# Optimization experiments

Measured on AMD Instinct MI355X. Metric: run time of the kernel, lower is better.

## Reference

```python
import jax, jax.numpy as jnp
import numpy as np

B, C, IMG = 128, 3, 224
P = 16
NP = (IMG // P) ** 2          # 196 patches
S = 1 + NP                    # 197 tokens
D = 384
HEADS = 6
HD = D // HEADS               # 64
DEPTH = 12
HID = 4 * D                   # 1536
NCLS = 100
PATCH_DIM = C * P * P         # 768
EPS = 1e-5


def setup_inputs() -> dict:
    key = jax.random.key(0)
    ks = jax.random.split(key, 24)
    g = lambda k, shape, s=0.02: jax.random.normal(k, shape, dtype=jnp.float32) * s
    return {
        "x": jax.random.normal(ks[0], (B, C, IMG, IMG), dtype=jnp.float32),
        "patch_w": g(ks[1], (D, PATCH_DIM)),
        "patch_b": jnp.zeros((D,), jnp.float32),
        "cls_token": g(ks[2], (1, 1, D)),
        "pos_embed": g(ks[3], (1, S, D)),
        "ln1_g": jnp.ones((DEPTH, D), jnp.float32),
        "ln1_b": jnp.zeros((DEPTH, D), jnp.float32),
        "qkv_w": g(ks[4], (DEPTH, 3 * D, D)),
        "qkv_b": jnp.zeros((DEPTH, 3 * D), jnp.float32),
        "out_w": g(ks[5], (DEPTH, D, D)),
        "out_b": jnp.zeros((DEPTH, D), jnp.float32),
        "ln2_g": jnp.ones((DEPTH, D), jnp.float32),
        "ln2_b": jnp.zeros((DEPTH, D), jnp.float32),
        "fc1_w": g(ks[6], (DEPTH, HID, D)),
        "fc1_b": jnp.zeros((DEPTH, HID), jnp.float32),
        "fc2_w": g(ks[7], (DEPTH, D, HID)),
        "fc2_b": jnp.zeros((DEPTH, D), jnp.float32),
        "lnf_g": jnp.ones((D,), jnp.float32),
        "lnf_b": jnp.zeros((D,), jnp.float32),
        "head_w": g(ks[8], (NCLS, D)),
    }


def _ln(x, g, b):
    m = jnp.mean(x, axis=-1, keepdims=True)
    v = jnp.mean(jnp.square(x - m), axis=-1, keepdims=True)
    return (x - m) * jax.lax.rsqrt(v + EPS) * g + b


def reference(x, patch_w, patch_b, cls_token, pos_embed,
              ln1_g, ln1_b, qkv_w, qkv_b, out_w, out_b,
              ln2_g, ln2_b, fc1_w, fc1_b, fc2_w, fc2_b,
              lnf_g, lnf_b, head_w):
    b = x.shape[0]
    hp = IMG // P
    # patchify: unfold(2,P).unfold(3,P).permute(0,2,3,1,4,5) -> [B, N, C*P*P]
    patches = x.reshape(b, C, hp, P, hp, P).transpose(0, 2, 4, 1, 3, 5).reshape(b, NP, PATCH_DIM)
    tok = patches @ patch_w.T + patch_b                           # [B, NP, D]
    h = jnp.concatenate([jnp.broadcast_to(cls_token, (b, 1, D)), tok], axis=1)
    h = h + pos_embed[:, :S, :]
    scale = 1.0 / np.sqrt(HD).astype(np.float32)
    for i in range(DEPTH):
        xn = _ln(h, ln1_g[i], ln1_b[i])
        qkv = xn @ qkv_w[i].T + qkv_b[i]                          # [B, S, 3D]
        q, k, v = jnp.split(qkv, 3, axis=-1)
        q = q.reshape(b, S, HEADS, HD).transpose(0, 2, 1, 3) * scale
        k = k.reshape(b, S, HEADS, HD).transpose(0, 2, 1, 3)
        v = v.reshape(b, S, HEADS, HD).transpose(0, 2, 1, 3)
        attn = jax.nn.softmax(jnp.einsum('bhqd,bhkd->bhqk', q, k), axis=-1)
        ctx = jnp.einsum('bhqk,bhkd->bhqd', attn, v)
        ctx = ctx.transpose(0, 2, 1, 3).reshape(b, S, D)
        h = h + (ctx @ out_w[i].T + out_b[i])
        xn2 = _ln(h, ln2_g[i], ln2_b[i])
        hid = jax.nn.gelu(xn2 @ fc1_w[i].T + fc1_b[i], approximate=False)
        h = h + (hid @ fc2_w[i].T + fc2_b[i])
    cls = _ln(h[:, 0], lnf_g, lnf_b)
    return cls @ head_w.T                                         # [B, NCLS]
```

## Files before the change

### kernel.cpp

```cpp
#include <hip/hip_runtime.h>
#include <hip/hip_bf16.h>


#define S_ 197
#define D_ 384
#define BATCH 128

using bf16 = __hip_bfloat16;
typedef __attribute__((ext_vector_type(8))) __bf16 bf16x8;
typedef __attribute__((ext_vector_type(4))) float f32x4;

#if __has_builtin(__builtin_amdgcn_global_load_lds)
#define HAVE_GLL 1
__device__ __forceinline__ void gll16(const bf16* g, __bf16* l) {
  __builtin_amdgcn_global_load_lds(
      (const __attribute__((address_space(1))) void*)g,
      (__attribute__((address_space(3))) void*)l, 16, 0, 0);
}
#else
#define HAVE_GLL 0
#endif

__global__ __launch_bounds__(256) void k_f2b(const float* __restrict__ src,
                                             bf16* __restrict__ dst, int n4) {
  int i = blockIdx.x * 256 + threadIdx.x;
  if (i >= n4) return;
  float4 v = ((const float4*)src)[i];
  bf16 o[4] = {__float2bfloat16(v.x), __float2bfloat16(v.y),
               __float2bfloat16(v.z), __float2bfloat16(v.w)};
  ((uint2*)dst)[i] = *(uint2*)o;
}

__global__ __launch_bounds__(256) void k_embed_init(const float* __restrict__ cls,
                                                    const float* __restrict__ pos,
                                                    float* __restrict__ h) {
  int idx = blockIdx.x * 256 + threadIdx.x;
  if (idx >= BATCH * S_ * D_) return;
  int d = idx % D_;
  int s = (idx / D_) % S_;
  float v = pos[s * D_ + d];
  if (s == 0) v += cls[d];
  h[idx] = v;
}

__global__ __launch_bounds__(256) void k_patchify(const float* __restrict__ x,
                                                  bf16* __restrict__ patches) {
  int idx = blockIdx.x * 256 + threadIdx.x;
  if (idx >= BATCH * 196 * 768) return;
  int f = idx % 768;
  int n = (idx / 768) % 196;
  int b = idx / (768 * 196);
  int c = f >> 8, rem = f & 255, dy = rem >> 4, dx = rem & 15;
  int py = n / 14, px = n % 14;
  patches[idx] = __float2bfloat16(
      x[(((size_t)b * 3 + c) * 224 + py * 16 + dy) * 224 + px * 16 + dx]);
}

template <int MODE>
__global__ __launch_bounds__(256, 6) void k_gemm(const bf16* __restrict__ X,
                                                 const bf16* __restrict__ W,
                                                 const float* __restrict__ bias,
                                                 bf16* __restrict__ out,
                                                 float* __restrict__ res,
                                                 int N, int K, int remap) {
  __shared__ __align__(16) __bf16 As[2][64 * 32];
  __shared__ __align__(16) __bf16 Bs[2][128 * 32];
  const int tid = threadIdx.x;
  const int m0 = blockIdx.y * 64, n0 = blockIdx.x * 128;
  const int lane = tid & 63, w = tid >> 6;
  const int l16 = lane & 15, quad = lane >> 4;
  f32x4 acc[4][2] = {};

  const int scol = (((lane & 3) ^ ((lane >> 3) & 3)) << 3);
  const bf16* Ag = X + (size_t)(m0 + w * 16 + (lane >> 2)) * K + scol;
  const bf16* Bg = W + (size_t)(n0 + w * 32 + (lane >> 2)) * K + scol;
  const int ldsA = w * 512;
  const int ldsB = w * 1024;

  const int jx8 = ((quad ^ ((l16 >> 1) & 3)) << 3);
  const int aoff = l16 * 32 + jx8;
  const int boff = (w * 32 + l16) * 32 + jx8;

#if HAVE_GLL
#define STAGE(buf, k0)                                       \
  do {                                                       \
    gll16(Ag + (k0), &As[buf][ldsA]);                        \
    gll16(Bg + (k0), &Bs[buf][ldsB]);                        \
    gll16(Bg + (k0) + (size_t)16 * K, &Bs[buf][ldsB + 512]); \
  } while (0)
#else
#define STAGE(buf, k0)                                                       \
  do {                                                                       \
    *(uint4*)(&As[buf][ldsA + (lane >> 2) * 32 + (lane & 3) * 8]) =          \
        *(const uint4*)(Ag + (k0) - scol + (lane & 3) * 8);                  \
    *(uint4*)(&Bs[buf][ldsB + (lane >> 2) * 32 + (lane & 3) * 8]) =          \
        *(const uint4*)(Bg + (k0) - scol + (lane & 3) * 8);                  \
    *(uint4*)(&Bs[buf][ldsB + 512 + (lane >> 2) * 32 + (lane & 3) * 8]) =    \
        *(const uint4*)(Bg + (k0) - scol + (size_t)16 * K + (lane & 3) * 8); \
  } while (0)
#endif

  STAGE(0, 0);
  __syncthreads();
  for (int k0 = 0; k0 < K; k0 += 32) {
    const int cb = (k0 >> 5) & 1;
    if (k0 + 32 < K) STAGE(cb ^ 1, k0 + 32);
    bf16x8 av[4], bv[2];
#pragma unroll
    for (int i = 0; i < 4; i++)
      av[i] = *(const bf16x8*)(&As[cb][aoff + i * 512]);
#pragma unroll
    for (int j = 0; j < 2; j++)
      bv[j] = *(const bf16x8*)(&Bs[cb][boff + j * 512]);
#pragma unroll
    for (int i = 0; i < 4; i++)
#pragma unroll
      for (int j = 0; j < 2; j++)
        acc[i][j] = __builtin_amdgcn_mfma_f32_16x16x32_bf16(av[i], bv[j], acc[i][j], 0, 0, 0);
    __syncthreads();
  }
#undef STAGE

  float bvv[2];
#pragma unroll
  for (int j = 0; j < 2; j++)
    bvv[j] = bias[n0 + w * 32 + j * 16 + l16];
#pragma unroll
  for (int i = 0; i < 4; i++) {
    const int rbase = m0 + i * 16 + quad * 4;
#pragma unroll
    for (int j = 0; j < 2; j++) {
      const int col = n0 + w * 32 + j * 16 + l16;
#pragma unroll
      for (int r = 0; r < 4; r++) {
        float v = acc[i][j][r] + bvv[j];
        int rw = rbase + r;
        if (MODE == 0) {
          out[(size_t)rw * N + col] = __float2bfloat16(v);
        } else if (MODE == 1) {
          float gl = 0.5f * v * (1.f + erff(v * 0.70710678118f));
          out[(size_t)rw * N + col] = __float2bfloat16(gl);
        } else {
          int hr = remap ? (rw + rw / 196 + 1) : rw;
          res[(size_t)hr * N + col] += v;
        }
      }
    }
  }
}

__global__ __launch_bounds__(128) void k_ln(const float* __restrict__ h,
                                            const float* __restrict__ g,
                                            const float* __restrict__ bt,
                                            bf16* __restrict__ xn) {
  const int r = blockIdx.x, t = threadIdx.x;
  const float* row = h + (size_t)r * D_;
  float x0 = row[t], x1 = row[t + 128], x2 = row[t + 256];
  float s = x0 + x1 + x2;
  float q = x0 * x0 + x1 * x1 + x2 * x2;
#pragma unroll
  for (int o = 32; o; o >>= 1) {
    s += __shfl_xor(s, o);
    q += __shfl_xor(q, o);
  }
  __shared__ float rs[2], rq[2];
  if ((t & 63) == 0) { rs[t >> 6] = s; rq[t >> 6] = q; }
  __syncthreads();
  s = rs[0] + rs[1];
  q = rq[0] + rq[1];
  const float mean = s * (1.f / 384.f);
  const float var = q * (1.f / 384.f) - mean * mean;
  const float rstd = rsqrtf(var + 1e-5f);
  bf16* o = xn + (size_t)r * D_;
  o[t] = __float2bfloat16((x0 - mean) * rstd * g[t] + bt[t]);
  o[t + 128] = __float2bfloat16((x1 - mean) * rstd * g[t + 128] + bt[t + 128]);
  o[t + 256] = __float2bfloat16((x2 - mean) * rstd * g[t + 256] + bt[t + 256]);
}

__global__ __launch_bounds__(256) void k_attn(const bf16* __restrict__ qkv,
                                              bf16* __restrict__ ctx) {
  const int bh = blockIdx.x;
  const int b = bh / 6, hd = bh % 6;
  const bf16* Qg = qkv + (size_t)b * S_ * 1152 + hd * 64;
  const bf16* Kg = Qg + 384;
  const bf16* Vg = Qg + 768;
  __shared__ __align__(16) __bf16 Vt[64 * 232];
  __shared__ __align__(16) __bf16 Ps[4][16 * 232];
  const int tid = threadIdx.x;
  const int lane = tid & 63, w = tid >> 6;
  const int l16 = lane & 15, quad = lane >> 4;
  const __bf16 z = (__bf16)0.0f;

  for (int i = tid; i < 64 * 35; i += 256) {
    int d = i / 35, k = 197 + i % 35;
    Vt[d * 232 + k] = z;
  }
  for (int i = tid; i < S_ * 64; i += 256) {
    int k = i >> 6, d = i & 63;
    Vt[d * 232 + k] = *(const __bf16*)&Vg[(size_t)k * 1152 + d];
  }
  for (int i = lane; i < 16 * 24; i += 64) {
    int r = i / 24, c = 208 + i % 24;
    Ps[w][r * 232 + c] = z;
  }
  __syncthreads();

  const bf16x8 zf = {};
  for (int band = w; band < 13; band += 4) {
    const int qrow = band * 16 + l16;
    bf16x8 aq0 = zf, aq1 = zf;
    if (qrow < S_) {
      aq0 = *(const bf16x8*)(Qg + (size_t)qrow * 1152 + quad * 8);
      aq1 = *(const bf16x8*)(Qg + (size_t)qrow * 1152 + 32 + quad * 8);
    }
    f32x4 sc[13];
#pragma unroll
    for (int t = 0; t < 13; t++) {
      const int krow = t * 16 + l16;
      bf16x8 bk0 = zf, bk1 = zf;
      if (krow < S_) {
        bk0 = *(const bf16x8*)(Kg + (size_t)krow * 1152 + quad * 8);
        bk1 = *(const bf16x8*)(Kg + (size_t)krow * 1152 + 32 + quad * 8);
      }
      f32x4 a = {};
      a = __builtin_amdgcn_mfma_f32_16x16x32_bf16(aq0, bk0, a, 0, 0, 0);
      a = __builtin_amdgcn_mfma_f32_16x16x32_bf16(aq1, bk1, a, 0, 0, 0);
      sc[t] = a;
    }
#pragma unroll
    for (int t = 0; t < 13; t++)
#pragma unroll
      for (int r = 0; r < 4; r++) sc[t][r] *= 0.125f;
    if (l16 >= 5) {
#pragma unroll
      for (int r = 0; r < 4; r++) sc[12][r] = -1e30f;
    }
    f32x4 mx = sc[0];
#pragma unroll
    for (int t = 1; t < 13; t++)
#pragma unroll
      for (int r = 0; r < 4; r++) mx[r] = fmaxf(mx[r], sc[t][r]);
#pragma unroll
    for (int o = 1; o < 16; o <<= 1)
#pragma unroll
      for (int r = 0; r < 4; r++) mx[r] = fmaxf(mx[r], __shfl_xor(mx[r], o));
    f32x4 sum = {};
#pragma unroll
    for (int t = 0; t < 13; t++)
#pragma unroll
      for (int r = 0; r < 4; r++) {
        float p = __expf(sc[t][r] - mx[r]);
        sc[t][r] = p;
        sum[r] += p;
      }
#pragma unroll
    for (int o = 1; o < 16; o <<= 1)
#pragma unroll
      for (int r = 0; r < 4; r++) sum[r] += __shfl_xor(sum[r], o);
    f32x4 rinv;
#pragma unroll
    for (int r = 0; r < 4; r++) rinv[r] = 1.0f / sum[r];
#pragma unroll
    for (int t = 0; t < 13; t++)
#pragma unroll
      for (int r = 0; r < 4; r++)
        Ps[w][(quad * 4 + r) * 232 + t * 16 + l16] = (__bf16)sc[t][r];
    f32x4 oacc[4] = {};
#pragma unroll
    for (int ks = 0; ks < 7; ks++) {
      bf16x8 pa = *(const bf16x8*)&Ps[w][l16 * 232 + ks * 32 + quad * 8];
#pragma unroll
      for (int c = 0; c < 4; c++) {
        bf16x8 bv = *(const bf16x8*)&Vt[(c * 16 + l16) * 232 + ks * 32 + quad * 8];
        oacc[c] = __builtin_amdgcn_mfma_f32_16x16x32_bf16(pa, bv, oacc[c], 0, 0, 0);
      }
    }
    const int orow = band * 16 + quad * 4;
#pragma unroll
    for (int c = 0; c < 4; c++)
#pragma unroll
      for (int r = 0; r < 4; r++) {
        const int rw = orow + r;
        if (rw < S_)
          ctx[((size_t)b * S_ + rw) * D_ + hd * 64 + c * 16 + l16] =
              __float2bfloat16(oacc[c][r] * rinv[r]);
      }
  }
}

__global__ __launch_bounds__(128) void k_head(const float* __restrict__ h,
                                              const float* __restrict__ g,
                                              const float* __restrict__ bt,
                                              const float* __restrict__ hw,
                                              float* __restrict__ out) {
  const int b = blockIdx.x, t = threadIdx.x;
  const float* row = h + (size_t)b * S_ * D_;
  float x0 = row[t], x1 = row[t + 128], x2 = row[t + 256];
  float s = x0 + x1 + x2;
  float q = x0 * x0 + x1 * x1 + x2 * x2;
#pragma unroll
  for (int o = 32; o; o >>= 1) {
    s += __shfl_xor(s, o);
    q += __shfl_xor(q, o);
  }
  __shared__ float rs[2], rq[2];
  if ((t & 63) == 0) { rs[t >> 6] = s; rq[t >> 6] = q; }
  __syncthreads();
  s = rs[0] + rs[1];
  q = rq[0] + rq[1];
  const float mean = s * (1.f / 384.f);
  const float var = q * (1.f / 384.f) - mean * mean;
  const float rstd = rsqrtf(var + 1e-5f);
  __shared__ float clsn[384];
  clsn[t] = (x0 - mean) * rstd * g[t] + bt[t];
  clsn[t + 128] = (x1 - mean) * rstd * g[t + 128] + bt[t + 128];
  clsn[t + 256] = (x2 - mean) * rstd * g[t + 256] + bt[t + 256];
  __syncthreads();
  if (t < 100) {
    const float* wr = hw + (size_t)t * D_;
    float a = 0.f;
    for (int d = 0; d < 384; d++) a += clsn[d] * wr[d];
    out[b * 100 + t] = a;
  }
}

extern "C" void kernel_launch(void* const* d_in, const int* in_sizes, int n_in,
                              void* d_out, int out_size, void* d_ws, size_t ws_size,
                              hipStream_t stream) {
  (void)in_sizes; (void)n_in; (void)out_size; (void)ws_size;
  const float* x       = (const float*)d_in[0];
  const float* patch_w = (const float*)d_in[1];
  const float* patch_b = (const float*)d_in[2];
  const float* cls_tok = (const float*)d_in[3];
  const float* pos_emb = (const float*)d_in[4];
  const float* ln1_g   = (const float*)d_in[5];
  const float* ln1_b   = (const float*)d_in[6];
  const float* qkv_w   = (const float*)d_in[7];
  const float* qkv_b   = (const float*)d_in[8];
  const float* out_w   = (const float*)d_in[9];
  const float* out_b   = (const float*)d_in[10];
  const float* ln2_g   = (const float*)d_in[11];
  const float* ln2_b   = (const float*)d_in[12];
  const float* fc1_w   = (const float*)d_in[13];
  const float* fc1_b   = (const float*)d_in[14];
  const float* fc2_w   = (const float*)d_in[15];
  const float* fc2_b   = (const float*)d_in[16];
  const float* lnf_g   = (const float*)d_in[17];
  const float* lnf_b   = (const float*)d_in[18];
  const float* head_w  = (const float*)d_in[19];
  float* out = (float*)d_out;

  const size_t R = (size_t)BATCH * S_;
  char* p = (char*)d_ws;
  float* h  = (float*)p; p += R * 384 * 4;
  bf16* xn  = (bf16*)p;  p += R * 384 * 2;
  bf16* u   = (bf16*)p;  p += R * 1536 * 2;
  bf16* qkvb = u;
  bf16* ctxb = u + R * 1152;
  bf16* hidb = u;
  bf16* patches = u;
  bf16* wb  = (bf16*)p;
  bf16* patch_wb = wb;
  bf16* qkv_wb   = patch_wb + 294912;
  bf16* out_wb   = qkv_wb + 5308416;
  bf16* fc1_wb   = out_wb + 1769472;
  bf16* fc2_wb   = fc1_wb + 7077888;

  k_f2b<<<dim3((294912 / 4 + 255) / 256), dim3(256), 0, stream>>>(patch_w, patch_wb, 294912 / 4);
  k_f2b<<<dim3((5308416 / 4 + 255) / 256), dim3(256), 0, stream>>>(qkv_w, qkv_wb, 5308416 / 4);
  k_f2b<<<dim3((1769472 / 4 + 255) / 256), dim3(256), 0, stream>>>(out_w, out_wb, 1769472 / 4);
  k_f2b<<<dim3((7077888 / 4 + 255) / 256), dim3(256), 0, stream>>>(fc1_w, fc1_wb, 7077888 / 4);
  k_f2b<<<dim3((7077888 / 4 + 255) / 256), dim3(256), 0, stream>>>(fc2_w, fc2_wb, 7077888 / 4);

  k_embed_init<<<dim3((BATCH * S_ * D_) / 256), dim3(256), 0, stream>>>(cls_tok, pos_emb, h);
  k_patchify<<<dim3((BATCH * 196 * 768) / 256), dim3(256), 0, stream>>>(x, patches);
  k_gemm<2><<<dim3(3, 392), dim3(256), 0, stream>>>(patches, patch_wb, patch_b, nullptr, h, 384, 768, 1);

  for (int i = 0; i < 12; i++) {
    k_ln<<<dim3((unsigned)R), dim3(128), 0, stream>>>(h, ln1_g + i * 384, ln1_b + i * 384, xn);
    k_gemm<0><<<dim3(9, 394), dim3(256), 0, stream>>>(xn, qkv_wb + (size_t)i * 1152 * 384,
                                                      qkv_b + i * 1152, qkvb, nullptr, 1152, 384, 0);
    k_attn<<<dim3(768), dim3(256), 0, stream>>>(qkvb, ctxb);
    k_gemm<2><<<dim3(3, 394), dim3(256), 0, stream>>>(ctxb, out_wb + (size_t)i * 384 * 384,
                                                      out_b + i * 384, nullptr, h, 384, 384, 0);
    k_ln<<<dim3((unsigned)R), dim3(128), 0, stream>>>(h, ln2_g + i * 384, ln2_b + i * 384, xn);
    k_gemm<1><<<dim3(12, 394), dim3(256), 0, stream>>>(xn, fc1_wb + (size_t)i * 1536 * 384,
                                                       fc1_b + i * 1536, hidb, nullptr, 1536, 384, 0);
    k_gemm<2><<<dim3(3, 394), dim3(256), 0, stream>>>(hidb, fc2_wb + (size_t)i * 384 * 1536,
                                                      fc2_b + i * 384, nullptr, h, 384, 1536, 0);
  }
  k_head<<<dim3(128), dim3(128), 0, stream>>>(h, lnf_g, lnf_b, head_w, out);
}
```

Before: 3.808 ms.

## Stage A tile in 384-wide K phases and read weights directly from global

The GEMM kernel now loads a whole 64x384 activation panel into LDS per phase, with one barrier per phase instead of double-buffered 32-wide K steps. Weight (B) fragments are read straight from global memory into registers instead of being staged through shared memory. K becomes a template parameter so the loop is fully unrolled. This cuts barrier count and LDS traffic for B, at the cost of more LDS per block (48KB), lower occupancy (launch bounds 3) and uncoalesced, unhidden global loads for weights.

```diff
diff --git a/kernel.cpp b/kernel.cpp
--- a/kernel.cpp
+++ b/kernel.cpp
@@ -56,15 +56,15 @@
       x[(((size_t)b * 3 + c) * 224 + py * 16 + dy) * 224 + px * 16 + dx]);
 }
 
-template <int MODE>
-__global__ __launch_bounds__(256, 6) void k_gemm(const bf16* __restrict__ X,
+template <int MODE, int KK>
+__global__ __launch_bounds__(256, 3) void k_gemm(const bf16* __restrict__ X,
                                                  const bf16* __restrict__ W,
                                                  const float* __restrict__ bias,
                                                  bf16* __restrict__ out,
                                                  float* __restrict__ res,
-                                                 int N, int K, int remap) {
-  __shared__ __align__(16) __bf16 As[2][64 * 32];
-  __shared__ __align__(16) __bf16 Bs[2][128 * 32];
+                                                 int N, int remap) {
+  constexpr int PH = KK / 384;
+  __shared__ __align__(16) __bf16 As[12 * 2048];
   const int tid = threadIdx.x;
   const int m0 = blockIdx.y * 64, n0 = blockIdx.x * 128;
   const int lane = tid & 63, w = tid >> 6;
@@ -72,54 +72,39 @@
   f32x4 acc[4][2] = {};
 
   const int scol = (((lane & 3) ^ ((lane >> 3) & 3)) << 3);
-  const bf16* Ag = X + (size_t)(m0 + w * 16 + (lane >> 2)) * K + scol;
-  const bf16* Bg = W + (size_t)(n0 + w * 32 + (lane >> 2)) * K + scol;
-  const int ldsA = w * 512;
-  const int ldsB = w * 1024;
-
+  const bf16* Ag = X + (size_t)(m0 + w * 16 + (lane >> 2)) * KK + scol;
   const int jx8 = ((quad ^ ((l16 >> 1) & 3)) << 3);
-  const int aoff = l16 * 32 + jx8;
-  const int boff = (w * 32 + l16) * 32 + jx8;
-
+  const bf16* Bg0 = W + (size_t)(n0 + w * 32 + l16) * KK + quad * 8;
+  const bf16* Bg1 = Bg0 + (size_t)16 * KK;
+
+  for (int ph = 0; ph < PH; ph++) {
+    if (ph) __syncthreads();
+#pragma unroll
+    for (int s = 0; s < 12; s++) {
 #if HAVE_GLL
-#define STAGE(buf, k0)                                       \
-  do {                                                       \
-    gll16(Ag + (k0), &As[buf][ldsA]);                        \
-    gll16(Bg + (k0), &Bs[buf][ldsB]);                        \
-    gll16(Bg + (k0) + (size_t)16 * K, &Bs[buf][ldsB + 512]); \
-  } while (0)
+      gll16(Ag + ph * 384 + s * 32, &As[s * 2048 + w * 512]);
 #else
-#define STAGE(buf, k0)                                                       \
-  do {                                                                       \
-    *(uint4*)(&As[buf][ldsA + (lane >> 2) * 32 + (lane & 3) * 8]) =          \
-        *(const uint4*)(Ag + (k0) - scol + (lane & 3) * 8);                  \
-    *(uint4*)(&Bs[buf][ldsB + (lane >> 2) * 32 + (lane & 3) * 8]) =          \
-        *(const uint4*)(Bg + (k0) - scol + (lane & 3) * 8);                  \
-    *(uint4*)(&Bs[buf][ldsB + 512 + (lane >> 2) * 32 + (lane & 3) * 8]) =    \
-        *(const uint4*)(Bg + (k0) - scol + (size_t)16 * K + (lane & 3) * 8); \
-  } while (0)
+      *(uint4*)(&As[s * 2048 + w * 512 + lane * 8]) =
+          *(const uint4*)(Ag + ph * 384 + s * 32);
 #endif
-
-  STAGE(0, 0);
-  __syncthreads();
-  for (int k0 = 0; k0 < K; k0 += 32) {
-    const int cb = (k0 >> 5) & 1;
-    if (k0 + 32 < K) STAGE(cb ^ 1, k0 + 32);
-    bf16x8 av[4], bv[2];
-#pragma unroll
-    for (int i = 0; i < 4; i++)
-      av[i] = *(const bf16x8*)(&As[cb][aoff + i * 512]);
-#pragma unroll
-    for (int j = 0; j < 2; j++)
-      bv[j] = *(const bf16x8*)(&Bs[cb][boff + j * 512]);
-#pragma unroll
-    for (int i = 0; i < 4; i++)
-#pragma unroll
-      for (int j = 0; j < 2; j++)
-        acc[i][j] = __builtin_amdgcn_mfma_f32_16x16x32_bf16(av[i], bv[j], acc[i][j], 0, 0, 0);
+    }
     __syncthreads();
-  }
-#undef STAGE
+#pragma unroll
+    for (int s = 0; s < 12; s++) {
+      const int kk = ph * 384 + s * 32;
+      bf16x8 bv0 = *(const bf16x8*)(Bg0 + kk);
+      bf16x8 bv1 = *(const bf16x8*)(Bg1 + kk);
+      bf16x8 av[4];
+#pragma unroll
+      for (int i = 0; i < 4; i++)
+        av[i] = *(const bf16x8*)(&As[s * 2048 + (i * 16 + l16) * 32 + jx8]);
+#pragma unroll
+      for (int i = 0; i < 4; i++) {
+        acc[i][0] = __builtin_amdgcn_mfma_f32_16x16x32_bf16(av[i], bv0, acc[i][0], 0, 0, 0);
+        acc[i][1] = __builtin_amdgcn_mfma_f32_16x16x32_bf16(av[i], bv1, acc[i][1], 0, 0, 0);
+      }
+    }
+  }
 
   float bvv[2];
 #pragma unroll
@@ -374,20 +359,20 @@
 
   k_embed_init<<<dim3((BATCH * S_ * D_) / 256), dim3(256), 0, stream>>>(cls_tok, pos_emb, h);
   k_patchify<<<dim3((BATCH * 196 * 768) / 256), dim3(256), 0, stream>>>(x, patches);
-  k_gemm<2><<<dim3(3, 392), dim3(256), 0, stream>>>(patches, patch_wb, patch_b, nullptr, h, 384, 768, 1);
+  k_gemm<2, 768><<<dim3(3, 392), dim3(256), 0, stream>>>(patches, patch_wb, patch_b, nullptr, h, 384, 1);
 
   for (int i = 0; i < 12; i++) {
     k_ln<<<dim3((unsigned)R), dim3(128), 0, stream>>>(h, ln1_g + i * 384, ln1_b + i * 384, xn);
-    k_gemm<0><<<dim3(9, 394), dim3(256), 0, stream>>>(xn, qkv_wb + (size_t)i * 1152 * 384,
-                                                      qkv_b + i * 1152, qkvb, nullptr, 1152, 384, 0);
+    k_gemm<0, 384><<<dim3(9, 394), dim3(256), 0, stream>>>(xn, qkv_wb + (size_t)i * 1152 * 384,
+                                                           qkv_b + i * 1152, qkvb, nullptr, 1152, 0);
     k_attn<<<dim3(768), dim3(256), 0, stream>>>(qkvb, ctxb);
-    k_gemm<2><<<dim3(3, 394), dim3(256), 0, stream>>>(ctxb, out_wb + (size_t)i * 384 * 384,
-                                                      out_b + i * 384, nullptr, h, 384, 384, 0);
+    k_gemm<2, 384><<<dim3(3, 394), dim3(256), 0, stream>>>(ctxb, out_wb + (size_t)i * 384 * 384,
+                                                           out_b + i * 384, nullptr, h, 384, 0);
     k_ln<<<dim3((unsigned)R), dim3(128), 0, stream>>>(h, ln2_g + i * 384, ln2_b + i * 384, xn);
-    k_gemm<1><<<dim3(12, 394), dim3(256), 0, stream>>>(xn, fc1_wb + (size_t)i * 1536 * 384,
-                                                       fc1_b + i * 1536, hidb, nullptr, 1536, 384, 0);
-    k_gemm<2><<<dim3(3, 394), dim3(256), 0, stream>>>(hidb, fc2_wb + (size_t)i * 384 * 1536,
-                                                      fc2_b + i * 384, nullptr, h, 384, 1536, 0);
+    k_gemm<1, 384><<<dim3(12, 394), dim3(256), 0, stream>>>(xn, fc1_wb + (size_t)i * 1536 * 384,
+                                                            fc1_b + i * 1536, hidb, nullptr, 1536, 0);
+    k_gemm<2, 1536><<<dim3(3, 394), dim3(256), 0, stream>>>(hidb, fc2_wb + (size_t)i * 384 * 1536,
+                                                            fc2_b + i * 384, nullptr, h, 384, 0);
   }
   k_head<<<dim3(128), dim3(128), 0, stream>>>(h, lnf_g, lnf_b, head_w, out);
 }
```

Measured after the change: 4.476 ms. +17.5%, slower.
